# Kernel optimization log

Measured on AMD Instinct MI355X. Metric: run time of the kernel, lower is better.

Reference implementation:

```python
import jax, jax.numpy as jnp
import numpy as np

NUM_CLASSES = 8192
FEAT_DIM = 64
BATCH = 16384
LAMB = 0.01
LAMB1 = 10.0


def setup_inputs() -> dict:
    key = jax.random.key(0)
    k1, k2, k3 = jax.random.split(key, 3)
    y = jax.random.randint(k1, (BATCH,), 0, NUM_CLASSES, dtype=jnp.int64 if jax.config.jax_enable_x64 else jnp.int32)
    feat = jax.random.normal(k2, (BATCH, FEAT_DIM), dtype=jnp.float32)
    centers = jax.random.normal(k3, (NUM_CLASSES, FEAT_DIM), dtype=jnp.float32)
    return {"y": y, "feat": feat, "centers": centers}


def reference(y, feat, centers):
    B = feat.shape[0]
    K = centers.shape[0]
    # center loss: 0.5 * ||feat - centers[y]||^2 / B
    diff = feat - centers[y]
    loss_cen = 0.5 * jnp.sum(diff * diff) / B
    # pairwise angular loss: sum_{i != j} C[i] . sg(C[j]) / (sg(|C_i|) sg(|C_j|)) + 1
    # (original uses .data for second operand and for norms -> stop_gradient)
    c_sg = jax.lax.stop_gradient(centers)
    dist = jnp.sqrt(jnp.sum(c_sg * c_sg, axis=1))  # [K]
    G = centers @ c_sg.T                            # [K, K]
    cos = G / (dist[:, None] * dist[None, :])
    off_diag = 1.0 - jnp.eye(K, dtype=cos.dtype)
    loss_ang = jnp.sum(cos * off_diag) + K * (K - 1)  # the '+1' per off-diag pair
    return LAMB * (loss_cen + LAMB1 * loss_ang)
```

## Files before the change

### kernel.cpp

```cpp
#include <hip/hip_runtime.h>
#include <hip/hip_bf16.h>

#define KCLS 8192
#define DFEAT 64
#define BATCH_N 16384
#define LAMB 0.01
#define LAMB1 10.0

constexpr int NBLK_C = 128;
constexpr int NBLK_B = 256;

__global__ __launch_bounds__(256) void illoss_fused(const int* __restrict__ y,
                                                    const float* __restrict__ feat,
                                                    const float* __restrict__ centers,
                                                    float* __restrict__ ws) {
    const int tid  = threadIdx.x;
    const int lane = tid & 63;
    const int wave = tid >> 6;
    const int blk  = blockIdx.x;
    const float4* __restrict__ centers4 = (const float4*)centers;

    __shared__ float sacc[4][16][4];
    __shared__ float wacc[4];

    if (blk < NBLK_C) {
        const int gwid = blk * 4 + wave;
        float ax = 0.f, ay = 0.f, az = 0.f, aw = 0.f;
        #pragma unroll
        for (int it = 0; it < 4; ++it) {
            const int row0 = gwid * 16 + it * 4;
            float4 v = centers4[row0 * 16 + lane];
            float ss = v.x * v.x + v.y * v.y + v.z * v.z + v.w * v.w;
            ss += __shfl_xor(ss, 1, 64);
            ss += __shfl_xor(ss, 2, 64);
            ss += __shfl_xor(ss, 4, 64);
            ss += __shfl_xor(ss, 8, 64);
            float inv = __frsqrt_rn(ss);
            ax += v.x * inv; ay += v.y * inv; az += v.z * inv; aw += v.w * inv;
        }
        ax += __shfl_xor(ax, 16, 64); ay += __shfl_xor(ay, 16, 64);
        az += __shfl_xor(az, 16, 64); aw += __shfl_xor(aw, 16, 64);
        ax += __shfl_xor(ax, 32, 64); ay += __shfl_xor(ay, 32, 64);
        az += __shfl_xor(az, 32, 64); aw += __shfl_xor(aw, 32, 64);
        if (lane < 16) {
            sacc[wave][lane][0] = ax; sacc[wave][lane][1] = ay;
            sacc[wave][lane][2] = az; sacc[wave][lane][3] = aw;
        }
        __syncthreads();
        if (tid < 64) {
            const int c = tid;
            float s = sacc[0][c >> 2][c & 3] + sacc[1][c >> 2][c & 3]
                    + sacc[2][c >> 2][c & 3] + sacc[3][c >> 2][c & 3];
            ws[blk * 64 + c] = s;
        }
    } else {
        const int bblk = blk - NBLK_C;
        const int gwid = bblk * 4 + wave;
        const int base = gwid * 16;
        const float4* __restrict__ feat4 = (const float4*)feat;
        int cls[4];
        #pragma unroll
        for (int it = 0; it < 4; ++it) cls[it] = y[base + it * 4 + (lane >> 4)];
        float acc = 0.f;
        #pragma unroll
        for (int it = 0; it < 4; ++it) {
            float4 f = feat4[(base + it * 4) * 16 + lane];
            float4 c = centers4[cls[it] * 16 + (lane & 15)];
            float dx = f.x - c.x, dy = f.y - c.y, dz = f.z - c.z, dw = f.w - c.w;
            acc += dx * dx + dy * dy + dz * dz + dw * dw;
        }
        acc += __shfl_xor(acc, 1, 64);
        acc += __shfl_xor(acc, 2, 64);
        acc += __shfl_xor(acc, 4, 64);
        acc += __shfl_xor(acc, 8, 64);
        acc += __shfl_xor(acc, 16, 64);
        acc += __shfl_xor(acc, 32, 64);
        if (lane == 0) wacc[wave] = acc;
        __syncthreads();
        if (tid == 0) ws[NBLK_C * 64 + bblk] = wacc[0] + wacc[1] + wacc[2] + wacc[3];
    }
}

__global__ __launch_bounds__(64) void illoss_final(const float* __restrict__ ws,
                                                   float* __restrict__ out) {
    const int lane = threadIdx.x;
    float s0 = 0.f, s1 = 0.f, s2a = 0.f, s3 = 0.f;
    #pragma unroll
    for (int b = 0; b < NBLK_C; b += 4) {
        s0 += ws[(b + 0) * 64 + lane];
        s1 += ws[(b + 1) * 64 + lane];
        s2a += ws[(b + 2) * 64 + lane];
        s3 += ws[(b + 3) * 64 + lane];
    }
    float S = (s0 + s1) + (s2a + s3);
    float s2 = S * S;
    s2 += __shfl_xor(s2, 1, 64);
    s2 += __shfl_xor(s2, 2, 64);
    s2 += __shfl_xor(s2, 4, 64);
    s2 += __shfl_xor(s2, 8, 64);
    s2 += __shfl_xor(s2, 16, 64);
    s2 += __shfl_xor(s2, 32, 64);
    const float* cw = ws + NBLK_C * 64;
    float cacc = cw[lane] + cw[lane + 64] + cw[lane + 128] + cw[lane + 192];
    cacc += __shfl_xor(cacc, 1, 64);
    cacc += __shfl_xor(cacc, 2, 64);
    cacc += __shfl_xor(cacc, 4, 64);
    cacc += __shfl_xor(cacc, 8, 64);
    cacc += __shfl_xor(cacc, 16, 64);
    cacc += __shfl_xor(cacc, 32, 64);
    if (lane == 0) {
        double loss_cen = 0.5 * (double)cacc / (double)BATCH_N;
        double loss_ang = (double)s2 - (double)KCLS + (double)KCLS * (double)(KCLS - 1);
        out[0] = (float)(LAMB * (loss_cen + LAMB1 * loss_ang));
    }
}

extern "C" void kernel_launch(void* const* d_in, const int* in_sizes, int n_in,
                              void* d_out, int out_size, void* d_ws, size_t ws_size,
                              hipStream_t stream) {
    const int*   y       = (const int*)d_in[0];
    const float* feat    = (const float*)d_in[1];
    const float* centers = (const float*)d_in[2];
    float* out = (float*)d_out;
    float* ws  = (float*)d_ws;

    illoss_fused<<<NBLK_C + NBLK_B, 256, 0, stream>>>(y, feat, centers, ws);
    illoss_final<<<1, 64, 0, stream>>>(ws, out);
}
```

Before: 11.70 us.

## Merge both phases and final reduction into one cooperative kernel with grid sync

Replaces the two-kernel launch (a role-split fused kernel plus a single-block final reduction) with one cooperative kernel of 256 blocks. Each block now does both the center-normalization partial sums and the center-loss partial sums, then a grid-wide sync lets block 0 compute the final loss. This is meant to remove the second launch and the inter-kernel gap. In exchange it adds the cost of a cooperative launch and a grid barrier.

```diff
diff --git a/kernel.cpp b/kernel.cpp
--- a/kernel.cpp
+++ b/kernel.cpp
@@ -1,5 +1,8 @@
 #include <hip/hip_runtime.h>
 #include <hip/hip_bf16.h>
+#include <hip/hip_cooperative_groups.h>
+
+namespace cg = cooperative_groups;
 
 #define KCLS 8192
 #define DFEAT 64
@@ -7,111 +10,109 @@
 #define LAMB 0.01
 #define LAMB1 10.0
 
-constexpr int NBLK_C = 128;
-constexpr int NBLK_B = 256;
+constexpr int NBLK = 256;
 
-__global__ __launch_bounds__(256) void illoss_fused(const int* __restrict__ y,
-                                                    const float* __restrict__ feat,
-                                                    const float* __restrict__ centers,
-                                                    float* __restrict__ ws) {
+__global__ __launch_bounds__(256) void illoss_coop(const int* __restrict__ y,
+                                                   const float* __restrict__ feat,
+                                                   const float* __restrict__ centers,
+                                                   float* __restrict__ ws,
+                                                   float* __restrict__ out) {
     const int tid  = threadIdx.x;
     const int lane = tid & 63;
     const int wave = tid >> 6;
     const int blk  = blockIdx.x;
+    const int gwid = blk * 4 + wave;
     const float4* __restrict__ centers4 = (const float4*)centers;
+    const float4* __restrict__ feat4    = (const float4*)feat;
 
     __shared__ float sacc[4][16][4];
     __shared__ float wacc[4];
+    __shared__ float fin[4][64];
 
-    if (blk < NBLK_C) {
-        const int gwid = blk * 4 + wave;
-        float ax = 0.f, ay = 0.f, az = 0.f, aw = 0.f;
-        #pragma unroll
-        for (int it = 0; it < 4; ++it) {
-            const int row0 = gwid * 16 + it * 4;
-            float4 v = centers4[row0 * 16 + lane];
-            float ss = v.x * v.x + v.y * v.y + v.z * v.z + v.w * v.w;
-            ss += __shfl_xor(ss, 1, 64);
-            ss += __shfl_xor(ss, 2, 64);
-            ss += __shfl_xor(ss, 4, 64);
-            ss += __shfl_xor(ss, 8, 64);
-            float inv = __frsqrt_rn(ss);
-            ax += v.x * inv; ay += v.y * inv; az += v.z * inv; aw += v.w * inv;
+    const int base = gwid * 16;
+    int cls[4];
+    #pragma unroll
+    for (int it = 0; it < 4; ++it) cls[it] = y[base + it * 4 + (lane >> 4)];
+
+    float ax = 0.f, ay = 0.f, az = 0.f, aw = 0.f;
+    #pragma unroll
+    for (int it = 0; it < 2; ++it) {
+        const int row0 = gwid * 8 + it * 4;
+        float4 v = centers4[row0 * 16 + lane];
+        float ss = v.x * v.x + v.y * v.y + v.z * v.z + v.w * v.w;
+        ss += __shfl_xor(ss, 1, 64);
+        ss += __shfl_xor(ss, 2, 64);
+        ss += __shfl_xor(ss, 4, 64);
+        ss += __shfl_xor(ss, 8, 64);
+        float inv = __frsqrt_rn(ss);
+        ax += v.x * inv; ay += v.y * inv; az += v.z * inv; aw += v.w * inv;
+    }
+    ax += __shfl_xor(ax, 16, 64); ay += __shfl_xor(ay, 16, 64);
+    az += __shfl_xor(az, 16, 64); aw += __shfl_xor(aw, 16, 64);
+    ax += __shfl_xor(ax, 32, 64); ay += __shfl_xor(ay, 32, 64);
+    az += __shfl_xor(az, 32, 64); aw += __shfl_xor(aw, 32, 64);
+    if (lane < 16) {
+        sacc[wave][lane][0] = ax; sacc[wave][lane][1] = ay;
+        sacc[wave][lane][2] = az; sacc[wave][lane][3] = aw;
+    }
+
+    float acc = 0.f;
+    #pragma unroll
+    for (int it = 0; it < 4; ++it) {
+        float4 f = feat4[(base + it * 4) * 16 + lane];
+        float4 c = centers4[cls[it] * 16 + (lane & 15)];
+        float dx = f.x - c.x, dy = f.y - c.y, dz = f.z - c.z, dw = f.w - c.w;
+        acc += dx * dx + dy * dy + dz * dz + dw * dw;
+    }
+    acc += __shfl_xor(acc, 1, 64);
+    acc += __shfl_xor(acc, 2, 64);
+    acc += __shfl_xor(acc, 4, 64);
+    acc += __shfl_xor(acc, 8, 64);
+    acc += __shfl_xor(acc, 16, 64);
+    acc += __shfl_xor(acc, 32, 64);
+    if (lane == 0) wacc[wave] = acc;
+    __syncthreads();
+
+    if (tid < 64) {
+        const int c = tid;
+        float s = sacc[0][c >> 2][c & 3] + sacc[1][c >> 2][c & 3]
+                + sacc[2][c >> 2][c & 3] + sacc[3][c >> 2][c & 3];
+        ws[blk * 64 + c] = s;
+    }
+    if (tid == 0) ws[NBLK * 64 + blk] = wacc[0] + wacc[1] + wacc[2] + wacc[3];
+
+    cg::this_grid().sync();
+
+    if (blk == 0) {
+        const int c = tid & 63, w = tid >> 6;
+        float s = 0.f;
+        #pragma unroll 8
+        for (int b = w; b < NBLK; b += 4) s += ws[b * 64 + c];
+        fin[w][c] = s;
+        __syncthreads();
+        if (wave == 0) {
+            float S = fin[0][lane] + fin[1][lane] + fin[2][lane] + fin[3][lane];
+            float s2 = S * S;
+            s2 += __shfl_xor(s2, 1, 64);
+            s2 += __shfl_xor(s2, 2, 64);
+            s2 += __shfl_xor(s2, 4, 64);
+            s2 += __shfl_xor(s2, 8, 64);
+            s2 += __shfl_xor(s2, 16, 64);
+            s2 += __shfl_xor(s2, 32, 64);
+            const float* cw = ws + NBLK * 64;
+            float cacc = cw[lane] + cw[lane + 64] + cw[lane + 128] + cw[lane + 192];
+            cacc += __shfl_xor(cacc, 1, 64);
+            cacc += __shfl_xor(cacc, 2, 64);
+            cacc += __shfl_xor(cacc, 4, 64);
+            cacc += __shfl_xor(cacc, 8, 64);
+            cacc += __shfl_xor(cacc, 16, 64);
+            cacc += __shfl_xor(cacc, 32, 64);
+            if (lane == 0) {
+                double loss_cen = 0.5 * (double)cacc / (double)BATCH_N;
+                double loss_ang = (double)s2 - (double)KCLS + (double)KCLS * (double)(KCLS - 1);
+                out[0] = (float)(LAMB * (loss_cen + LAMB1 * loss_ang));
+            }
         }
-        ax += __shfl_xor(ax, 16, 64); ay += __shfl_xor(ay, 16, 64);
-        az += __shfl_xor(az, 16, 64); aw += __shfl_xor(aw, 16, 64);
-        ax += __shfl_xor(ax, 32, 64); ay += __shfl_xor(ay, 32, 64);
-        az += __shfl_xor(az, 32, 64); aw += __shfl_xor(aw, 32, 64);
-        if (lane < 16) {
-            sacc[wave][lane][0] = ax; sacc[wave][lane][1] = ay;
-            sacc[wave][lane][2] = az; sacc[wave][lane][3] = aw;
-        }
-        __syncthreads();
-        if (tid < 64) {
-            const int c = tid;
-            float s = sacc[0][c >> 2][c & 3] + sacc[1][c >> 2][c & 3]
-                    + sacc[2][c >> 2][c & 3] + sacc[3][c >> 2][c & 3];
-            ws[blk * 64 + c] = s;
-        }
-    } else {
-        const int bblk = blk - NBLK_C;
-        const int gwid = bblk * 4 + wave;
-        const int base = gwid * 16;
-        const float4* __restrict__ feat4 = (const float4*)feat;
-        int cls[4];
-        #pragma unroll
-        for (int it = 0; it < 4; ++it) cls[it] = y[base + it * 4 + (lane >> 4)];
-        float acc = 0.f;
-        #pragma unroll
-        for (int it = 0; it < 4; ++it) {
-            float4 f = feat4[(base + it * 4) * 16 + lane];
-            float4 c = centers4[cls[it] * 16 + (lane & 15)];
-            float dx = f.x - c.x, dy = f.y - c.y, dz = f.z - c.z, dw = f.w - c.w;
-            acc += dx * dx + dy * dy + dz * dz + dw * dw;
-        }
-        acc += __shfl_xor(acc, 1, 64);
-        acc += __shfl_xor(acc, 2, 64);
-        acc += __shfl_xor(acc, 4, 64);
-        acc += __shfl_xor(acc, 8, 64);
-        acc += __shfl_xor(acc, 16, 64);
-        acc += __shfl_xor(acc, 32, 64);
-        if (lane == 0) wacc[wave] = acc;
-        __syncthreads();
-        if (tid == 0) ws[NBLK_C * 64 + bblk] = wacc[0] + wacc[1] + wacc[2] + wacc[3];
-    }
-}
-
-__global__ __launch_bounds__(64) void illoss_final(const float* __restrict__ ws,
-                                                   float* __restrict__ out) {
-    const int lane = threadIdx.x;
-    float s0 = 0.f, s1 = 0.f, s2a = 0.f, s3 = 0.f;
-    #pragma unroll
-    for (int b = 0; b < NBLK_C; b += 4) {
-        s0 += ws[(b + 0) * 64 + lane];
-        s1 += ws[(b + 1) * 64 + lane];
-        s2a += ws[(b + 2) * 64 + lane];
-        s3 += ws[(b + 3) * 64 + lane];
-    }
-    float S = (s0 + s1) + (s2a + s3);
-    float s2 = S * S;
-    s2 += __shfl_xor(s2, 1, 64);
-    s2 += __shfl_xor(s2, 2, 64);
-    s2 += __shfl_xor(s2, 4, 64);
-    s2 += __shfl_xor(s2, 8, 64);
-    s2 += __shfl_xor(s2, 16, 64);
-    s2 += __shfl_xor(s2, 32, 64);
-    const float* cw = ws + NBLK_C * 64;
-    float cacc = cw[lane] + cw[lane + 64] + cw[lane + 128] + cw[lane + 192];
-    cacc += __shfl_xor(cacc, 1, 64);
-    cacc += __shfl_xor(cacc, 2, 64);
-    cacc += __shfl_xor(cacc, 4, 64);
-    cacc += __shfl_xor(cacc, 8, 64);
-    cacc += __shfl_xor(cacc, 16, 64);
-    cacc += __shfl_xor(cacc, 32, 64);
-    if (lane == 0) {
-        double loss_cen = 0.5 * (double)cacc / (double)BATCH_N;
-        double loss_ang = (double)s2 - (double)KCLS + (double)KCLS * (double)(KCLS - 1);
-        out[0] = (float)(LAMB * (loss_cen + LAMB1 * loss_ang));
     }
 }
 
@@ -124,6 +125,6 @@
     float* out = (float*)d_out;
     float* ws  = (float*)d_ws;
 
-    illoss_fused<<<NBLK_C + NBLK_B, 256, 0, stream>>>(y, feat, centers, ws);
-    illoss_final<<<1, 64, 0, stream>>>(ws, out);
+    void* args[] = {(void*)&y, (void*)&feat, (void*)&centers, (void*)&ws, (void*)&out};
+    hipLaunchCooperativeKernel((void*)illoss_coop, dim3(NBLK), dim3(256), args, 0, stream);
 }
```

Result: slower. 40.69 us (+247.6%).
